# Kernel optimization log

Measured on AMD Instinct MI355X. Metric: run time of the kernel, lower is better.

Reference implementation:

```python
import jax, jax.numpy as jnp
import numpy as np
import math

B, S, HID, H, D = 8, 1024, 1024, 16, 64
MAX_POS = 1024  # max_position_embeddings


def setup_inputs() -> dict:
    key = jax.random.key(0)
    ks = jax.random.split(key, 8)
    sc = 1.0 / math.sqrt(HID)
    return {
        "hidden_states": jax.random.normal(ks[0], (B, S, HID), jnp.float32),
        "Wq": jax.random.normal(ks[1], (HID, HID), jnp.float32) * sc,
        "bq": jnp.zeros((HID,), jnp.float32),
        "Wk": jax.random.normal(ks[2], (HID, HID), jnp.float32) * sc,
        "bk": jnp.zeros((HID,), jnp.float32),
        "Wv": jax.random.normal(ks[3], (HID, HID), jnp.float32) * sc,
        "bv": jnp.zeros((HID,), jnp.float32),
        "dist_table": jax.random.normal(ks[4], (2 * MAX_POS - 1, D), jnp.float32) * 0.02,
    }


def _heads(x):
    # [B,S,HID] -> [B,H,S,D]
    return x.reshape(B, S, H, D).transpose(0, 2, 1, 3)


def reference(hidden_states, Wq, bq, Wk, bk, Wv, bv, dist_table):
    q = _heads(hidden_states @ Wq + bq)            # [B,H,S,D]
    k = _heads(hidden_states @ Wk + bk)            # [B,H,S,D]
    # NOTE: source bug — value_layer uses the key projection in self-attention path.
    v = _heads(hidden_states @ Wk + bk)            # [B,H,S,D]

    scores = jnp.einsum("bhld,bhrd->bhlr", q, k)   # [B,H,S,S]

    # relative_key_query positional bias
    pos = jnp.arange(S)
    distance = pos[:, None] - pos[None, :]          # [S,S] in [-(S-1), S-1]
    pos_emb = dist_table[distance + MAX_POS - 1]    # [S,S,D]
    rel_q = jnp.einsum("bhld,lrd->bhlr", q, pos_emb)
    rel_k = jnp.einsum("bhrd,lrd->bhlr", k, pos_emb)
    scores = (scores + rel_q + rel_k) / math.sqrt(D)

    probs = jax.nn.softmax(scores, axis=-1)         # dropout is identity at inference
    ctx = jnp.einsum("bhlr,bhrd->bhld", probs, v)   # [B,H,S,D]
    ctx = ctx.transpose(0, 2, 1, 3).reshape(B, S, HID)
    return ctx
```

## Files before the change

### kernel.cpp

```cpp
#include <hip/hip_runtime.h>
#include <hip/hip_bf16.h>


typedef float  f32x4 __attribute__((ext_vector_type(4)));
typedef short  s16x8 __attribute__((ext_vector_type(8)));
typedef unsigned short u16x4 __attribute__((ext_vector_type(4)));
typedef unsigned int   u32x4 __attribute__((ext_vector_type(4)));

#define MFMA16(a,b,c) __builtin_amdgcn_mfma_f32_16x16x32_bf16((a),(b),(c),0,0,0)

static __device__ __forceinline__ unsigned short f2b(float x){
    unsigned int u = __float_as_uint(x);
    unsigned int r = (u + 0x7fffu + ((u >> 16) & 1u)) >> 16;
    return (unsigned short)r;
}
static __device__ __forceinline__ float b2f(unsigned short b){
    return __uint_as_float(((unsigned int)b) << 16);
}
static __device__ __forceinline__ unsigned int cvtpk(float a, float b){
#if defined(__has_builtin) && __has_builtin(__builtin_amdgcn_cvt_pk_bf16_f32)
    typedef __bf16 bf16x2_t __attribute__((ext_vector_type(2)));
    bf16x2_t v = __builtin_amdgcn_cvt_pk_bf16_f32(a, b);
    unsigned int u; __builtin_memcpy(&u, &v, 4); return u;
#else
    return (unsigned int)f2b(a) | ((unsigned int)f2b(b) << 16);
#endif
}
static __device__ __forceinline__ void gl_lds16(const unsigned short* g, unsigned short* l){
    __builtin_amdgcn_global_load_lds(
        (const __attribute__((address_space(1))) unsigned int*)g,
        (__attribute__((address_space(3))) unsigned int*)l, 16, 0, 0);
}

__global__ void prep_table(const float* __restrict__ T, unsigned short* __restrict__ Tb){
    int i = blockIdx.x * 256 + threadIdx.x;
    if (i < 2047 * 64)      Tb[i] = f2b(T[i]);
    else if (i < 2048 * 64) Tb[i] = 0;
}

__global__ __launch_bounds__(256)
void prep_a(const float* __restrict__ Hs,
            unsigned short* __restrict__ Ahi, unsigned short* __restrict__ Alo){
    int i = (blockIdx.x * 256 + threadIdx.x) * 8;
    float v[8];
    *(f32x4*)&v[0] = *(const f32x4*)(Hs + i);
    *(f32x4*)&v[4] = *(const f32x4*)(Hs + i + 4);
    unsigned short h8[8] __attribute__((aligned(16)));
    unsigned short l8[8] __attribute__((aligned(16)));
#pragma unroll
    for (int j = 0; j < 8; j++) {
        unsigned short h = f2b(v[j]);
        h8[j] = h;
        l8[j] = f2b(v[j] - b2f(h));
    }
    *(s16x8*)&Ahi[i] = *(s16x8*)h8;
    *(s16x8*)&Alo[i] = *(s16x8*)l8;
}

__global__ __launch_bounds__(256)
void prep_w(const float* __restrict__ Wq, const float* __restrict__ Wk,
            unsigned short* __restrict__ WqThi, unsigned short* __restrict__ WqTlo,
            unsigned short* __restrict__ WkThi, unsigned short* __restrict__ WkTlo){
    __shared__ unsigned short LH[64][72];
    __shared__ unsigned short LL[64][72];
    const int bx = blockIdx.x;
    const float* W = (bx & 1) ? Wk : Wq;
    unsigned short* Thi = (bx & 1) ? WkThi : WqThi;
    unsigned short* Tlo = (bx & 1) ? WkTlo : WqTlo;
    const int tile = bx >> 1;
    const int k0 = (tile >> 4) * 64, n0 = (tile & 15) * 64;
    const int t = threadIdx.x;
    const int r = t >> 3, c8 = (t & 7) * 8;
#pragma unroll
    for (int half = 0; half < 2; half++) {
        int rr = r + half * 32;
        const float* p = W + (size_t)(k0 + rr) * 1024 + n0 + c8;
        float v[8];
        *(f32x4*)&v[0] = *(const f32x4*)p;
        *(f32x4*)&v[4] = *(const f32x4*)(p + 4);
#pragma unroll
        for (int j = 0; j < 8; j++) {
            unsigned short h = f2b(v[j]);
            LH[rr][c8 + j] = h;
            LL[rr][c8 + j] = f2b(v[j] - b2f(h));
        }
    }
    __syncthreads();
    const int n = t >> 2, kg = (t & 3) * 16;
    unsigned short oh[16] __attribute__((aligned(16)));
    unsigned short ol[16] __attribute__((aligned(16)));
#pragma unroll
    for (int j = 0; j < 16; j++) { oh[j] = LH[kg + j][n]; ol[j] = LL[kg + j][n]; }
    unsigned short* dh = Thi + (size_t)(n0 + n) * 1024 + k0 + kg;
    unsigned short* dl = Tlo + (size_t)(n0 + n) * 1024 + k0 + kg;
    *(s16x8*)dh       = *(s16x8*)&oh[0];
    *(s16x8*)(dh + 8) = *(s16x8*)&oh[8];
    *(s16x8*)dl       = *(s16x8*)&ol[0];
    *(s16x8*)(dl + 8) = *(s16x8*)&ol[8];
}

__global__ __launch_bounds__(512, 4)
void proj_gemm(const unsigned short* __restrict__ Ahi, const unsigned short* __restrict__ Alo,
               const unsigned short* __restrict__ WqThi, const unsigned short* __restrict__ WqTlo,
               const unsigned short* __restrict__ WkThi, const unsigned short* __restrict__ WkTlo,
               const float* __restrict__ bq, const float* __restrict__ bk,
               unsigned short* __restrict__ qbf, unsigned short* __restrict__ kbf,
               unsigned short* __restrict__ kTbf)
{
    __shared__ __attribute__((aligned(16))) unsigned short SL[16384];

    const int t = threadIdx.x, lane = t & 63, w = t >> 6;
    const int q4 = lane >> 4, l15 = lane & 15;
    const int wm = w >> 1, wn = w & 1;
    const int ntile = blockIdx.x & 15, mtile = blockIdx.x >> 4;
    const int m0 = mtile * 128, cn0 = (ntile & 7) * 128;
    const unsigned short* Bh = (ntile < 8) ? WqThi : WkThi;
    const unsigned short* Bl = (ntile < 8) ? WqTlo : WkTlo;

    f32x4 acc[2][4];
#pragma unroll
    for (int i = 0; i < 2; i++)
#pragma unroll
        for (int j = 0; j < 4; j++) acc[i][j] = (f32x4){0.f, 0.f, 0.f, 0.f};

    const int lr = lane >> 2, lc = (lane & 3) * 8;

    for (int kk0 = 0; kk0 < 1024; kk0 += 32) {
        __syncthreads();
#pragma unroll
        for (int i = 0; i < 4; i++) {
            const int seg = w * 4 + i;
            const int tid = seg >> 3, row0 = (seg & 7) * 16;
            const unsigned short* g;
            if      (tid == 0) g = Ahi + (size_t)(m0 + row0 + lr) * 1024 + kk0 + lc;
            else if (tid == 1) g = Alo + (size_t)(m0 + row0 + lr) * 1024 + kk0 + lc;
            else if (tid == 2) g = Bh  + (size_t)(cn0 + row0 + lr) * 1024 + kk0 + lc;
            else               g = Bl  + (size_t)(cn0 + row0 + lr) * 1024 + kk0 + lc;
            gl_lds16(g, &SL[seg * 512]);
        }
        __syncthreads();

        s16x8 ah[2], al[2], bh8[4], bl8[4];
#pragma unroll
        for (int sm = 0; sm < 2; sm++) {
            int r = wm * 32 + sm * 16 + l15;
            ah[sm] = *(const s16x8*)&SL[r * 32 + q4 * 8];
            al[sm] = *(const s16x8*)&SL[4096 + r * 32 + q4 * 8];
        }
#pragma unroll
        for (int sn = 0; sn < 4; sn++) {
            int r = wn * 64 + sn * 16 + l15;
            bh8[sn] = *(const s16x8*)&SL[8192 + r * 32 + q4 * 8];
            bl8[sn] = *(const s16x8*)&SL[12288 + r * 32 + q4 * 8];
        }
#pragma unroll
        for (int sm = 0; sm < 2; sm++)
#pragma unroll
            for (int sn = 0; sn < 4; sn++) {
                f32x4 a = acc[sm][sn];
                a = MFMA16(ah[sm], bh8[sn], a);
                a = MFMA16(ah[sm], bl8[sn], a);
                a = MFMA16(al[sm], bh8[sn], a);
                acc[sm][sn] = a;
            }
    }

#pragma unroll
    for (int sm = 0; sm < 2; sm++) {
#pragma unroll
        for (int sn = 0; sn < 4; sn++) {
            const int coln = ntile * 128 + wn * 64 + sn * 16 + l15;
            const float bias = (ntile < 8) ? bq[coln] : bk[coln - 1024];
            const int mbase = m0 + wm * 32 + sm * 16 + q4 * 4;
            const int bb = mbase >> 10, ss0 = mbase & 1023;
            unsigned short vb[4];
#pragma unroll
            for (int reg = 0; reg < 4; reg++) vb[reg] = f2b(acc[sm][sn][reg] + bias);
            if (ntile < 8) {
                const int hh = coln >> 6, d = coln & 63;
#pragma unroll
                for (int reg = 0; reg < 4; reg++)
                    qbf[(((size_t)(bb * 16 + hh) * 1024) + ss0 + reg) * 64 + d] = vb[reg];
            } else {
                const int ck = coln - 1024;
                const int hh = ck >> 6, d = ck & 63;
#pragma unroll
                for (int reg = 0; reg < 4; reg++)
                    kbf[(((size_t)(bb * 16 + hh) * 1024) + ss0 + reg) * 64 + d] = vb[reg];
                u16x4 pk = { vb[0], vb[1], vb[2], vb[3] };
                *(u16x4*)&kTbf[(((size_t)(bb * 16 + hh) * 64) + d) * 1024 + ss0] = pk;
            }
        }
    }
}

__global__ __launch_bounds__(512, 4)
void attn(const unsigned short* __restrict__ qbf, const unsigned short* __restrict__ kbf,
          const unsigned short* __restrict__ kTbf, const unsigned short* __restrict__ Tbf,
          float* __restrict__ out)
{
    __shared__ __attribute__((aligned(16))) unsigned char LDSRAW[59392];
    unsigned short* Klds = (unsigned short*)LDSRAW;
    unsigned short* Tlds = (unsigned short*)(LDSRAW + 8192);
    unsigned int*   GqS  = (unsigned int*)(LDSRAW + 32768);
    unsigned short* Pw   = (unsigned short*)(LDSRAW + 43008);
    float*          Ep   = (float*)LDSRAW;

    const int t = threadIdx.x;
    const int lane = t & 63, w = t >> 6;
    const int q4 = lane >> 4, l15 = lane & 15;
    const int swz8 = (l15 & 7) * 8;
    const int bh = blockIdx.x & 127;
    const int lb = (blockIdx.x >> 7) * 128;
    const int l0w = lb + w * 16;

    const unsigned short* qb = qbf + (size_t)bh * 65536;
    const unsigned short* kb = kbf + (size_t)bh * 65536;
    const unsigned short* kT = kTbf + (size_t)bh * 65536;

    const s16x8 qf0 = *(const s16x8*)(qb + (l0w + l15) * 64 + q4 * 8);
    const s16x8 qf1 = *(const s16x8*)(qb + (l0w + l15) * 64 + 32 + q4 * 8);

    const int dj_r = lane >> 3;
    const int dj_c = ((lane & 7) ^ dj_r) * 8;

#pragma unroll
    for (int i = 0; i < 4; i++) {
        const int seg = w * 4 + i;
        if (seg < 24) {
            const unsigned short* g = Tbf + (size_t)(lb + 960 + seg * 8 + dj_r) * 64 + dj_c;
            gl_lds16(g, Tlds + seg * 512);
        } else {
            const int s = seg - 24;
            const unsigned short* g = kb + (size_t)(s * 8 + dj_r) * 64 + dj_c;
            gl_lds16(g, Klds + s * 512);
        }
    }
    __syncthreads();

    f32x4 pacc[4];
#pragma unroll
    for (int n = 0; n < 4; n++) pacc[n] = (f32x4){0.f, 0.f, 0.f, 0.f};
    float psum = 0.f;

    unsigned int*   GqW = GqS + w * 320;
    unsigned short* PwW = Pw + w * 1024;

    const int pB0 = 64 + w * 16 + l15;
    s16x8 tb0 = *(const s16x8*)&Tlds[pB0 * 64 + ((q4 * 8) ^ swz8)];
    s16x8 tb1 = *(const s16x8*)&Tlds[pB0 * 64 + ((32 + q4 * 8) ^ swz8)];

    int r0 = 0;
    for (int c = 0; c < 16; c++) {
        s16x8 vf[4][2];
#pragma unroll
        for (int n = 0; n < 4; n++) {
            const unsigned short* vp = kT + (size_t)(n * 16 + l15) * 1024 + r0;
            vf[n][0] = *(const s16x8*)(vp + q4 * 8);
            vf[n][1] = *(const s16x8*)(vp + 32 + q4 * 8);
        }

        const int base = 1008 - 64 * c + w * 16;
#pragma unroll
        for (int rs = 0; rs < 4; rs++) {
            const int krow = rs * 16 + l15;
            const s16x8 kf0 = *(const s16x8*)&Klds[krow * 64 + ((q4 * 8) ^ swz8)];
            const s16x8 kf1 = *(const s16x8*)&Klds[krow * 64 + ((32 + q4 * 8) ^ swz8)];

            const int p0 = (base - rs * 16) % 192;
            int pa = p0 + l15; if (pa >= 192) pa -= 192;
            const s16x8 ta0 = *(const s16x8*)&Tlds[pa * 64 + ((q4 * 8) ^ swz8)];
            const s16x8 ta1 = *(const s16x8*)&Tlds[pa * 64 + ((32 + q4 * 8) ^ swz8)];

            f32x4 s = (f32x4){0.f, 0.f, 0.f, 0.f};
            s = MFMA16(kf0, qf0, s);
            s = MFMA16(kf1, qf1, s);

            f32x4 gq0 = (f32x4){0.f,0.f,0.f,0.f}, gq1 = (f32x4){0.f,0.f,0.f,0.f};
            f32x4 hk0 = (f32x4){0.f,0.f,0.f,0.f}, hk1 = (f32x4){0.f,0.f,0.f,0.f};
            gq0 = MFMA16(qf0, ta0, gq0); gq0 = MFMA16(qf1, ta1, gq0);
            gq1 = MFMA16(qf0, tb0, gq1); gq1 = MFMA16(qf1, tb1, gq1);
            hk0 = MFMA16(kf0, ta0, hk0); hk0 = MFMA16(kf1, ta1, hk0);
            hk1 = MFMA16(kf0, tb0, hk1); hk1 = MFMA16(kf1, tb1, hk1);

            u32x4 gpk;
#pragma unroll
            for (int reg = 0; reg < 4; reg++) gpk[reg] = cvtpk(gq0[reg], gq1[reg]);
            *(u32x4*)&GqW[l15 * 20 + q4 * 4] = gpk;

            const int n4b = l15 - q4 * 4 + 15;
            float pr[4];
#pragma unroll
            for (int reg = 0; reg < 4; reg++) {
                const int n4 = n4b - reg;
                const int srclane = (n4 & 15) | (lane & 48);
                const unsigned int hpk = cvtpk(hk0[reg], hk1[reg]);
                const unsigned int gsh = (unsigned int)__shfl((int)hpk, srclane);
                const unsigned int rkb = (n4 < 16) ? (gsh << 16) : (gsh & 0xffff0000u);
                const unsigned int gq  = GqW[(n4 & 15) * 20 + l15];
                const unsigned int rqb = (n4 < 16) ? (gq << 16) : (gq & 0xffff0000u);
                float sc = (s[reg] + __uint_as_float(rqb) + __uint_as_float(rkb)) * 0.125f - 4.0f;
                float p = __expf(sc);
                psum += p;
                pr[reg] = p;
            }
            unsigned int u0 = cvtpk(pr[0], pr[1]);
            unsigned int u1 = cvtpk(pr[2], pr[3]);
            unsigned long long pk2 = (unsigned long long)u0 | ((unsigned long long)u1 << 32);
            *(unsigned long long*)&PwW[l15 * 64 + ((rs * 16 + q4 * 4) ^ swz8)] = pk2;

            tb0 = ta0; tb1 = ta1;
        }

        const s16x8 pf0 = *(const s16x8*)&PwW[l15 * 64 + ((q4 * 8) ^ swz8)];
        const s16x8 pf1 = *(const s16x8*)&PwW[l15 * 64 + ((32 + q4 * 8) ^ swz8)];
#pragma unroll
        for (int n = 0; n < 4; n++) {
            pacc[n] = MFMA16(vf[n][0], pf0, pacc[n]);
            pacc[n] = MFMA16(vf[n][1], pf1, pacc[n]);
        }

        if (c < 15) {
            __syncthreads();
            const int cn = c + 1;
            {
                const unsigned short* g = kb + (size_t)(cn * 64 + w * 8 + dj_r) * 64 + dj_c;
                gl_lds16(g, Klds + w * 512);
            }
            {
                const int pnew = (1152 - 64 * cn) % 192;
                const unsigned short* g = Tbf + (size_t)(lb + 960 - 64 * cn + w * 8 + dj_r) * 64 + dj_c;
                gl_lds16(g, Tlds + pnew * 64 + w * 512);
            }
            __syncthreads();
        }
        r0 += 64;
    }

    psum += __shfl_xor(psum, 16);
    psum += __shfl_xor(psum, 32);
    const float inv = 1.0f / psum;

    __syncthreads();
    float* EpW = Ep + w * 1088;
#pragma unroll
    for (int n = 0; n < 4; n++) {
        f32x4 v = pacc[n];
        v[0] *= inv; v[1] *= inv; v[2] *= inv; v[3] *= inv;
        *(f32x4*)&EpW[l15 * 68 + n * 16 + q4 * 4] = v;
    }
    const int b0 = bh >> 4, hh = bh & 15;
    const int li = lane >> 2, gg = lane & 3;
#pragma unroll
    for (int cc = 0; cc < 4; cc++) {
        f32x4 v = *(const f32x4*)&EpW[li * 68 + gg * 16 + cc * 4];
        *(f32x4*)&out[((size_t)(b0 * 1024 + l0w + li) * 1024) + hh * 64 + gg * 16 + cc * 4] = v;
    }
}

extern "C" void kernel_launch(void* const* d_in, const int* in_sizes, int n_in,
                              void* d_out, int out_size, void* d_ws, size_t ws_size,
                              hipStream_t stream) {
    (void)in_sizes; (void)n_in; (void)out_size; (void)ws_size;
    const float* Hs = (const float*)d_in[0];
    const float* Wq = (const float*)d_in[1];
    const float* bq = (const float*)d_in[2];
    const float* Wk = (const float*)d_in[3];
    const float* bk = (const float*)d_in[4];
    const float* Tt = (const float*)d_in[7];
    float* out = (float*)d_out;

    unsigned short* qbf   = (unsigned short*)d_ws;
    unsigned short* kbf   = qbf  + (size_t)8 * 1024 * 1024;
    unsigned short* kTbf  = kbf  + (size_t)8 * 1024 * 1024;
    unsigned short* Tbf   = kTbf + (size_t)8 * 1024 * 1024;
    unsigned short* Ahi   = Tbf  + (size_t)2048 * 64;
    unsigned short* Alo   = Ahi  + (size_t)8 * 1024 * 1024;
    unsigned short* WqThi = Alo  + (size_t)8 * 1024 * 1024;
    unsigned short* WqTlo = WqThi + (size_t)1024 * 1024;
    unsigned short* WkThi = WqTlo + (size_t)1024 * 1024;
    unsigned short* WkTlo = WkThi + (size_t)1024 * 1024;

    hipLaunchKernelGGL(prep_table, dim3(512), dim3(256), 0, stream, Tt, Tbf);
    hipLaunchKernelGGL(prep_a, dim3(4096), dim3(256), 0, stream, Hs, Ahi, Alo);
    hipLaunchKernelGGL(prep_w, dim3(512), dim3(256), 0, stream,
                       Wq, Wk, WqThi, WqTlo, WkThi, WkTlo);
    hipLaunchKernelGGL(proj_gemm, dim3(1024), dim3(512), 0, stream,
                       Ahi, Alo, WqThi, WqTlo, WkThi, WkTlo, bq, bk, qbf, kbf, kTbf);
    hipLaunchKernelGGL(attn, dim3(1024), dim3(512), 0, stream,
                       qbf, kbf, kTbf, Tbf, out);
}
```

Before: 392.3 us.

## Feed PV MFMA directly from registers, reuse Gq tile, shrink LDS for occupancy

The attention kernel no longer stages bf16 probabilities through a per-wave LDS tile. Each 16-column slice of P is fed straight from registers into a 16x16x16 bf16 MFMA, software-pipelined one step behind, and V fragments are loaded per step. The previous step's Gq result is carried over instead of being recomputed, which removes two MFMAs per step. Shuffle index math is hoisted and uses ds_bpermute, and exp is rewritten as an exp2 of an FMA. LDS drops from about 58 KB to 40 KB and launch bounds move to 8 waves-per-EU, trading possible register pressure and smaller global loads for higher occupancy.

```diff
diff --git a/kernel.cpp b/kernel.cpp
--- a/kernel.cpp
+++ b/kernel.cpp
@@ -4,10 +4,26 @@
 
 typedef float  f32x4 __attribute__((ext_vector_type(4)));
 typedef short  s16x8 __attribute__((ext_vector_type(8)));
+typedef short  s16x4 __attribute__((ext_vector_type(4)));
 typedef unsigned short u16x4 __attribute__((ext_vector_type(4)));
 typedef unsigned int   u32x4 __attribute__((ext_vector_type(4)));
 
 #define MFMA16(a,b,c) __builtin_amdgcn_mfma_f32_16x16x32_bf16((a),(b),(c),0,0,0)
+
+#if defined(__has_builtin)
+#if __has_builtin(__builtin_amdgcn_mfma_f32_16x16x16bf16_1k)
+#define PV_MFMA(a,b,c) __builtin_amdgcn_mfma_f32_16x16x16bf16_1k((a),(b),(c),0,0,0)
+#endif
+#endif
+#ifndef PV_MFMA
+static __device__ __forceinline__ f32x4 pv_mfma_fb(s16x4 a, s16x4 b, f32x4 c){
+    s16x4 z = 0;
+    s16x8 a8 = __builtin_shufflevector(a, z, 0,1,2,3,4,5,6,7);
+    s16x8 b8 = __builtin_shufflevector(b, z, 0,1,2,3,4,5,6,7);
+    return MFMA16(a8, b8, c);
+}
+#define PV_MFMA(a,b,c) pv_mfma_fb((a),(b),(c))
+#endif
 
 static __device__ __forceinline__ unsigned short f2b(float x){
     unsigned int u = __float_as_uint(x);
@@ -194,16 +210,15 @@
     }
 }
 
-__global__ __launch_bounds__(512, 4)
+__global__ __launch_bounds__(512, 8)
 void attn(const unsigned short* __restrict__ qbf, const unsigned short* __restrict__ kbf,
           const unsigned short* __restrict__ kTbf, const unsigned short* __restrict__ Tbf,
           float* __restrict__ out)
 {
-    __shared__ __attribute__((aligned(16))) unsigned char LDSRAW[59392];
+    __shared__ __attribute__((aligned(16))) unsigned char LDSRAW[40960];
     unsigned short* Klds = (unsigned short*)LDSRAW;
     unsigned short* Tlds = (unsigned short*)(LDSRAW + 8192);
     unsigned int*   GqS  = (unsigned int*)(LDSRAW + 32768);
-    unsigned short* Pw   = (unsigned short*)(LDSRAW + 43008);
     float*          Ep   = (float*)LDSRAW;
 
     const int t = threadIdx.x;
@@ -243,23 +258,27 @@
     for (int n = 0; n < 4; n++) pacc[n] = (f32x4){0.f, 0.f, 0.f, 0.f};
     float psum = 0.f;
 
-    unsigned int*   GqW = GqS + w * 320;
-    unsigned short* PwW = Pw + w * 1024;
+    unsigned int* GqW = GqS + w * 256;
+
+    int bpa[4], shk[4], gix[4];
+#pragma unroll
+    for (int reg = 0; reg < 4; reg++) {
+        const int n4 = l15 - q4 * 4 - reg + 15;
+        bpa[reg] = ((n4 & 15) | (lane & 48)) << 2;
+        shk[reg] = (n4 < 16) ? 16 : 0;
+        gix[reg] = (n4 & 15) * 16 + l15;
+    }
 
     const int pB0 = 64 + w * 16 + l15;
     s16x8 tb0 = *(const s16x8*)&Tlds[pB0 * 64 + ((q4 * 8) ^ swz8)];
     s16x8 tb1 = *(const s16x8*)&Tlds[pB0 * 64 + ((32 + q4 * 8) ^ swz8)];
-
+    f32x4 gqP = (f32x4){0.f, 0.f, 0.f, 0.f};
+    gqP = MFMA16(qf0, tb0, gqP);
+    gqP = MFMA16(qf1, tb1, gqP);
+
+    s16x4 pfP = 0;
     int r0 = 0;
     for (int c = 0; c < 16; c++) {
-        s16x8 vf[4][2];
-#pragma unroll
-        for (int n = 0; n < 4; n++) {
-            const unsigned short* vp = kT + (size_t)(n * 16 + l15) * 1024 + r0;
-            vf[n][0] = *(const s16x8*)(vp + q4 * 8);
-            vf[n][1] = *(const s16x8*)(vp + 32 + q4 * 8);
-        }
-
         const int base = 1008 - 64 * c + w * 16;
 #pragma unroll
         for (int rs = 0; rs < 4; rs++) {
@@ -272,52 +291,50 @@
             const s16x8 ta0 = *(const s16x8*)&Tlds[pa * 64 + ((q4 * 8) ^ swz8)];
             const s16x8 ta1 = *(const s16x8*)&Tlds[pa * 64 + ((32 + q4 * 8) ^ swz8)];
 
+            if (rs > 0 || c > 0) {
+                const int rP = r0 + rs * 16 - 16;
+#pragma unroll
+                for (int n = 0; n < 4; n++) {
+                    const s16x4 vfn = *(const s16x4*)(kT + (size_t)(n * 16 + l15) * 1024 + rP + q4 * 4);
+                    pacc[n] = PV_MFMA(vfn, pfP, pacc[n]);
+                }
+            }
+
             f32x4 s = (f32x4){0.f, 0.f, 0.f, 0.f};
             s = MFMA16(kf0, qf0, s);
             s = MFMA16(kf1, qf1, s);
 
-            f32x4 gq0 = (f32x4){0.f,0.f,0.f,0.f}, gq1 = (f32x4){0.f,0.f,0.f,0.f};
+            f32x4 gq  = (f32x4){0.f,0.f,0.f,0.f};
             f32x4 hk0 = (f32x4){0.f,0.f,0.f,0.f}, hk1 = (f32x4){0.f,0.f,0.f,0.f};
-            gq0 = MFMA16(qf0, ta0, gq0); gq0 = MFMA16(qf1, ta1, gq0);
-            gq1 = MFMA16(qf0, tb0, gq1); gq1 = MFMA16(qf1, tb1, gq1);
+            gq  = MFMA16(qf0, ta0, gq);  gq  = MFMA16(qf1, ta1, gq);
             hk0 = MFMA16(kf0, ta0, hk0); hk0 = MFMA16(kf1, ta1, hk0);
             hk1 = MFMA16(kf0, tb0, hk1); hk1 = MFMA16(kf1, tb1, hk1);
 
             u32x4 gpk;
 #pragma unroll
-            for (int reg = 0; reg < 4; reg++) gpk[reg] = cvtpk(gq0[reg], gq1[reg]);
-            *(u32x4*)&GqW[l15 * 20 + q4 * 4] = gpk;
-
-            const int n4b = l15 - q4 * 4 + 15;
+            for (int reg = 0; reg < 4; reg++) gpk[reg] = cvtpk(gq[reg], gqP[reg]);
+            *(u32x4*)&GqW[l15 * 16 + q4 * 4] = gpk;
+
             float pr[4];
 #pragma unroll
             for (int reg = 0; reg < 4; reg++) {
-                const int n4 = n4b - reg;
-                const int srclane = (n4 & 15) | (lane & 48);
                 const unsigned int hpk = cvtpk(hk0[reg], hk1[reg]);
-                const unsigned int gsh = (unsigned int)__shfl((int)hpk, srclane);
-                const unsigned int rkb = (n4 < 16) ? (gsh << 16) : (gsh & 0xffff0000u);
-                const unsigned int gq  = GqW[(n4 & 15) * 20 + l15];
-                const unsigned int rqb = (n4 < 16) ? (gq << 16) : (gq & 0xffff0000u);
-                float sc = (s[reg] + __uint_as_float(rqb) + __uint_as_float(rkb)) * 0.125f - 4.0f;
-                float p = __expf(sc);
+                const unsigned int gsh = (unsigned int)__builtin_amdgcn_ds_bpermute(bpa[reg], (int)hpk);
+                const float relk = __uint_as_float((gsh << shk[reg]) & 0xffff0000u);
+                const unsigned int g = GqW[gix[reg]];
+                const float relq = __uint_as_float((g << shk[reg]) & 0xffff0000u);
+                const float tt = s[reg] + relq + relk;
+                const float p = exp2f(__builtin_fmaf(tt, 0.18033688011f, -5.77078016356f));
                 psum += p;
                 pr[reg] = p;
             }
-            unsigned int u0 = cvtpk(pr[0], pr[1]);
-            unsigned int u1 = cvtpk(pr[2], pr[3]);
-            unsigned long long pk2 = (unsigned long long)u0 | ((unsigned long long)u1 << 32);
-            *(unsigned long long*)&PwW[l15 * 64 + ((rs * 16 + q4 * 4) ^ swz8)] = pk2;
-
-            tb0 = ta0; tb1 = ta1;
-        }
-
-        const s16x8 pf0 = *(const s16x8*)&PwW[l15 * 64 + ((q4 * 8) ^ swz8)];
-        const s16x8 pf1 = *(const s16x8*)&PwW[l15 * 64 + ((32 + q4 * 8) ^ swz8)];
-#pragma unroll
-        for (int n = 0; n < 4; n++) {
-            pacc[n] = MFMA16(vf[n][0], pf0, pacc[n]);
-            pacc[n] = MFMA16(vf[n][1], pf1, pacc[n]);
+            {
+                u32x4 tmp; tmp[0] = cvtpk(pr[0], pr[1]); tmp[1] = cvtpk(pr[2], pr[3]);
+                s16x4 pf; __builtin_memcpy(&pf, &tmp, 8);
+                pfP = pf;
+            }
+
+            tb0 = ta0; tb1 = ta1; gqP = gq;
         }
 
         if (c < 15) {
@@ -335,6 +352,13 @@
             __syncthreads();
         }
         r0 += 64;
+    }
+    {
+#pragma unroll
+        for (int n = 0; n < 4; n++) {
+            const s16x4 vfn = *(const s16x4*)(kT + (size_t)(n * 16 + l15) * 1024 + 1008 + q4 * 4);
+            pacc[n] = PV_MFMA(vfn, pfP, pacc[n]);
+        }
     }
 
     psum += __shfl_xor(psum, 16);
```

After: 1.495 ms. 281% more time.
